# Kernel optimization log

Measured on AMD Instinct MI355X. Metric: run time of the kernel, lower is better.

## Reference

```python
import jax, jax.numpy as jnp
import numpy as np

N = 100000   # nodes
E = 1600000  # edges
G = 256      # graphs in batch
IN = 128     # in_feats
H = 64       # h_feats


def _xavier(k, shape):
    fan_in, fan_out = shape
    lim = float(np.sqrt(6.0 / (fan_in + fan_out)))
    return jax.random.uniform(k, shape, jnp.float32, -lim, lim)


def setup_inputs() -> dict:
    key = jax.random.key(0)
    ks = jax.random.split(key, 12)
    x = jax.random.normal(ks[0], (N, IN), jnp.float32)
    src = jax.random.randint(ks[1], (E,), 0, N)
    dst = jax.random.randint(ks[2], (E,), 0, N)
    ew = jax.random.uniform(ks[3], (E,), jnp.float32)
    gid = jnp.sort(jax.random.randint(ks[4], (N,), 0, G))
    def lin(k, fi, fo):
        kw, kb = jax.random.split(k)
        lim = float(np.sqrt(1.0 / fi))
        return (jax.random.uniform(kw, (fi, fo), jnp.float32, -lim, lim),
                jax.random.uniform(kb, (fo,), jnp.float32, -lim, lim))
    W1 = _xavier(ks[5], (IN, H)); b1 = jnp.zeros((H,), jnp.float32)
    W2 = _xavier(ks[6], (H, H));  b2 = jnp.zeros((H,), jnp.float32)
    W3 = _xavier(ks[7], (H, H));  b3 = jnp.zeros((H,), jnp.float32)
    Dw1, Db1 = lin(ks[8], H, 16)
    Dw2, Db2 = lin(ks[9], 16, 8)
    Dw3, Db3 = lin(ks[10], 8, 1)
    return {"x": x, "src": src, "dst": dst, "ew": ew, "gid": gid,
            "W1": W1, "b1": b1, "W2": W2, "b2": b2, "W3": W3, "b3": b3,
            "Dw1": Dw1, "Db1": Db1, "Dw2": Dw2, "Db2": Db2, "Dw3": Dw3, "Db3": Db3}


def reference(x, src, dst, ew, gid, W1, b1, W2, b2, W3, b3,
              Dw1, Db1, Dw2, Db2, Dw3, Db3):
    n = x.shape[0]
    # DGL GraphConv norm='both': unweighted degrees, clamped to >= 1
    deg_out = jnp.zeros((n,), x.dtype).at[src].add(1.0)
    deg_in = jnp.zeros((n,), x.dtype).at[dst].add(1.0)
    ns = jax.lax.rsqrt(jnp.maximum(deg_out, 1.0))  # src-side norm
    nd = jax.lax.rsqrt(jnp.maximum(deg_in, 1.0))   # dst-side norm

    def conv(h, W, b):
        # apply weight first (in >= out), then gather-scale-scatter
        h = (h * ns[:, None]) @ W                      # [N, out]
        m = h[src] * ew[:, None]                       # [E, out] edge messages
        agg = jnp.zeros((n, W.shape[1]), h.dtype).at[dst].add(m)
        return agg * nd[:, None] + b

    h = jax.nn.relu(conv(x, W1, b1))
    h = jax.nn.relu(conv(h, W2, b2))
    h = jax.nn.relu(conv(h, W3, b3))

    # mean_nodes: per-graph mean pooling
    counts = jnp.zeros((G,), h.dtype).at[gid].add(1.0)
    pooled = jnp.zeros((G, h.shape[1]), h.dtype).at[gid].add(h)
    pooled = pooled / jnp.maximum(counts, 1.0)[:, None]

    h = jax.nn.relu(pooled @ Dw1 + Db1)
    h = jax.nn.relu(h @ Dw2 + Db2)
    return jax.nn.sigmoid(h @ Dw3 + Db3)  # [G, 1]
```

## Files before the change

### kernel.cpp

```cpp
#include <hip/hip_runtime.h>
#include <math.h>

#define N_NODES 100000
#define N_EDGES 1600000
#define G_GRAPHS 256
#define IN_F 128
#define H_F 64

#define SCAN_CH 1024

#define HB 40
#define HCHUNK (N_EDGES / HB)
#define NWORDS (N_NODES / 4)
#define HNODES 25000
#define HWORDS (HNODES / 4)
#define HR 4

typedef unsigned int uint_t;
typedef unsigned short ushort_t;
typedef unsigned char uchar_t;
typedef __attribute__((ext_vector_type(8))) short short8;
typedef __attribute__((ext_vector_type(4))) float floatx4;
typedef __attribute__((ext_vector_type(2))) float floatx2;

__device__ __forceinline__ ushort_t f2bf(float f) {
  uint_t u = __float_as_uint(f);
  uint_t r = (u + 0x7fffu + ((u >> 16) & 1u)) >> 16;
  return (ushort_t)r;
}
__device__ __forceinline__ float bflo(uint_t u) { return __uint_as_float(u << 16); }
__device__ __forceinline__ uchar_t f2fp8(float f) {
  return (uchar_t)(__builtin_amdgcn_cvt_pk_fp8_f32(f, f, 0, false) & 0xff);
}

__global__ __launch_bounds__(1024) void hist8_kernel(
    const int* __restrict__ src, const int* __restrict__ dst,
    uint_t* __restrict__ p8dst, uint_t* __restrict__ p8src,
    uchar_t* __restrict__ rank8) {
  __shared__ uint_t h[HWORDS];
  const int a = blockIdx.x / (HR * HB);
  const int rem = blockIdx.x % (HR * HB);
  const int r = rem / HB;
  const int b = rem % HB;
  const uint_t rbase = (uint_t)(r * HNODES);

  for (int i = threadIdx.x; i < HWORDS; i += 1024) h[i] = 0u;
  __syncthreads();

  const int e0 = b * HCHUNK;
  const int* keys = a ? src : dst;
  const uint4* k4 = (const uint4*)(keys + e0);
  if (a == 0) {
    for (int i = threadIdx.x; i < HCHUNK / 4; i += 1024) {
      uint4 v = k4[i];
      int e = e0 + i * 4;
      uint_t t, sh;
      t = v.x - rbase; if (t < (uint_t)HNODES) { sh = (t & 3u) * 8u; rank8[e]     = (uchar_t)(atomicAdd(&h[t >> 2], 1u << sh) >> sh); }
      t = v.y - rbase; if (t < (uint_t)HNODES) { sh = (t & 3u) * 8u; rank8[e + 1] = (uchar_t)(atomicAdd(&h[t >> 2], 1u << sh) >> sh); }
      t = v.z - rbase; if (t < (uint_t)HNODES) { sh = (t & 3u) * 8u; rank8[e + 2] = (uchar_t)(atomicAdd(&h[t >> 2], 1u << sh) >> sh); }
      t = v.w - rbase; if (t < (uint_t)HNODES) { sh = (t & 3u) * 8u; rank8[e + 3] = (uchar_t)(atomicAdd(&h[t >> 2], 1u << sh) >> sh); }
    }
  } else {
    for (int i = threadIdx.x; i < HCHUNK / 4; i += 1024) {
      uint4 v = k4[i];
      uint_t t;
      t = v.x - rbase; if (t < (uint_t)HNODES) atomicAdd(&h[t >> 2], 1u << ((t & 3u) * 8u));
      t = v.y - rbase; if (t < (uint_t)HNODES) atomicAdd(&h[t >> 2], 1u << ((t & 3u) * 8u));
      t = v.z - rbase; if (t < (uint_t)HNODES) atomicAdd(&h[t >> 2], 1u << ((t & 3u) * 8u));
      t = v.w - rbase; if (t < (uint_t)HNODES) atomicAdd(&h[t >> 2], 1u << ((t & 3u) * 8u));
    }
  }
  __syncthreads();

  uint_t* outp = (a ? p8src : p8dst) + (size_t)b * NWORDS + r * HWORDS;
  for (int i = threadIdx.x; i < HWORDS; i += 1024) outp[i] = h[i];
}

__global__ __launch_bounds__(256) void scanA_kernel(
    const uint_t* __restrict__ p8dst, float* __restrict__ nd,
    int* __restrict__ row_ptr, int* __restrict__ bsums) {
  __shared__ int ts[256];
  const int tid = threadIdx.x;
  const int nodebase = blockIdx.x * SCAN_CH + tid * 4;
  const int w = nodebase >> 2;
  int c0 = 0, c1 = 0, c2 = 0, c3 = 0;
  if (nodebase < N_NODES) {
    for (int b = 0; b < HB; ++b) {
      uint_t x = p8dst[(size_t)b * NWORDS + w];
      c0 += (int)(x & 0xffu);
      c1 += (int)((x >> 8) & 0xffu);
      c2 += (int)((x >> 16) & 0xffu);
      c3 += (int)((x >> 24) & 0xffu);
    }
    ((float4*)nd)[w] = make_float4(
        rsqrtf(fmaxf((float)c0, 1.0f)), rsqrtf(fmaxf((float)c1, 1.0f)),
        rsqrtf(fmaxf((float)c2, 1.0f)), rsqrtf(fmaxf((float)c3, 1.0f)));
  }
  int s = c0 + c1 + c2 + c3;
  ts[tid] = s;
  __syncthreads();
  for (int off = 1; off < 256; off <<= 1) {
    int t = (tid >= off) ? ts[tid - off] : 0;
    __syncthreads();
    ts[tid] += t;
    __syncthreads();
  }
  int excl = (tid == 0) ? 0 : ts[tid - 1];
  if (nodebase < N_NODES)
    ((int4*)row_ptr)[w] = make_int4(excl, excl + c0, excl + c0 + c1,
                                    excl + c0 + c1 + c2);
  if (tid == 255) bsums[blockIdx.x] = ts[255];
}

__global__ __launch_bounds__(256) void scanB_kernel(int* __restrict__ bsums, int nb) {
  __shared__ int ts[256];
  const int tid = threadIdx.x;
  ts[tid] = (tid < nb) ? bsums[tid] : 0;
  __syncthreads();
  for (int off = 1; off < 256; off <<= 1) {
    int t = (tid >= off) ? ts[tid - off] : 0;
    __syncthreads();
    ts[tid] += t;
    __syncthreads();
  }
  if (tid < nb) bsums[tid] = (tid == 0) ? 0 : ts[tid - 1];
}

__global__ __launch_bounds__(256) void coff_kernel(
    const uint_t* __restrict__ p8dst, const int* __restrict__ bsums,
    const int* __restrict__ row_ptr, int* __restrict__ coff,
    int2* __restrict__ rc) {
  int v = blockIdx.x * blockDim.x + threadIdx.x;
  if (v >= N_NODES) return;
  int start = row_ptr[v] + bsums[v >> 10];
  int run = start;
  const int w = v >> 2, sh = (v & 3) * 8;
  for (int b = 0; b < HB; ++b) {
    int c = (int)((p8dst[(size_t)b * NWORDS + w] >> sh) & 0xffu);
    coff[(size_t)b * N_NODES + v] = run;
    run += c;
  }
  rc[v] = make_int2(start, run - start);
}

__global__ __launch_bounds__(256) void ns_kernel(
    const uint_t* __restrict__ p8src, float* __restrict__ ns) {
  int w = blockIdx.x * blockDim.x + threadIdx.x;
  if (w >= NWORDS) return;
  int c0 = 0, c1 = 0, c2 = 0, c3 = 0;
  for (int b = 0; b < HB; ++b) {
    uint_t x = p8src[(size_t)b * NWORDS + w];
    c0 += (int)(x & 0xffu);
    c1 += (int)((x >> 8) & 0xffu);
    c2 += (int)((x >> 16) & 0xffu);
    c3 += (int)((x >> 24) & 0xffu);
  }
  ((float4*)ns)[w] = make_float4(
      rsqrtf(fmaxf((float)c0, 1.0f)), rsqrtf(fmaxf((float)c1, 1.0f)),
      rsqrtf(fmaxf((float)c2, 1.0f)), rsqrtf(fmaxf((float)c3, 1.0f)));
}

#define PB 782
__global__ __launch_bounds__(256) void place_kernel(
    const int* __restrict__ src, const int* __restrict__ dst,
    const float* __restrict__ ew, const int* __restrict__ coff,
    const uchar_t* __restrict__ rank8, uint_t* __restrict__ csr) {
  int j = (blockIdx.x & 7) * PB + (blockIdx.x >> 3);
  int e = j * 256 + (int)threadIdx.x;
  if (e >= N_EDGES) return;
  int b = e / HCHUNK;
  int d = dst[e];
  int slot = coff[(size_t)b * N_NODES + d] + (int)rank8[e];
  uint_t entry = ((uint_t)(f2bf(ew[e]) & 0x7fff) << 17) | (uint_t)src[e];
  __builtin_nontemporal_store(entry, &csr[slot]);
}

template <int K, bool AFP32>
__global__ __launch_bounds__(256) void gemm_mfma_kernel(
    const void* __restrict__ Xin, const float* __restrict__ W,
    const float* __restrict__ ns, uchar_t* __restrict__ T, int ntiles) {
  constexpr int CH = K / 32;
  constexpr int WROW = K + 8;
  __shared__ __align__(16) ushort_t Wt[64 * WROW];
  const int tid = threadIdx.x;

  for (int i = tid; i < K * 64; i += 256) {
    int k = i >> 6, nn = i & 63;
    Wt[nn * WROW + k] = f2bf(W[i]);
  }
  __syncthreads();

  const int wave = tid >> 6;
  const int lane = tid & 63;
  const int tile = blockIdx.x * 4 + wave;
  if (tile >= ntiles) return;
  const int m = lane & 15;
  const int q = lane >> 4;
  const int node0 = tile * 16;

  short8 afrag[CH];
  if (AFP32) {
    const float* xr = (const float*)Xin + (size_t)(node0 + m) * K + q * 8;
#pragma unroll
    for (int c = 0; c < CH; ++c) {
      float4 xa = *(const float4*)(xr + c * 32);
      float4 xb = *(const float4*)(xr + c * 32 + 4);
      short8 a;
      a[0] = (short)f2bf(xa.x); a[1] = (short)f2bf(xa.y);
      a[2] = (short)f2bf(xa.z); a[3] = (short)f2bf(xa.w);
      a[4] = (short)f2bf(xb.x); a[5] = (short)f2bf(xb.y);
      a[6] = (short)f2bf(xb.z); a[7] = (short)f2bf(xb.w);
      afrag[c] = a;
    }
  } else {
    const ushort_t* xr = (const ushort_t*)Xin + (size_t)(node0 + m) * K + q * 8;
#pragma unroll
    for (int c = 0; c < CH; ++c)
      afrag[c] = *(const short8*)(xr + c * 32);
  }

  floatx4 acc[4];
#pragma unroll
  for (int t = 0; t < 4; ++t) acc[t] = (floatx4){0.f, 0.f, 0.f, 0.f};

#pragma unroll
  for (int t = 0; t < 4; ++t) {
    const ushort_t* wr = &Wt[(t * 16 + m) * WROW + q * 8];
#pragma unroll
    for (int c = 0; c < CH; ++c) {
      short8 bfrag = *(const short8*)(wr + c * 32);
      acc[t] = __builtin_amdgcn_mfma_f32_16x16x32_bf16(afrag[c], bfrag, acc[t], 0, 0, 0);
    }
  }

  float4 nsv = *(const float4*)(ns + node0 + q * 4);
  const float nsa[4] = {nsv.x, nsv.y, nsv.z, nsv.w};
#pragma unroll
  for (int t = 0; t < 4; ++t) {
#pragma unroll
    for (int r = 0; r < 4; ++r) {
      int node = node0 + q * 4 + r;
      T[(size_t)node * 64 + t * 16 + m] = f2fp8(acc[t][r] * nsa[r]);
    }
  }
}

__global__ __launch_bounds__(256) void gather_kernel(
    const uint_t* __restrict__ csr, const int2* __restrict__ rc,
    const uchar_t* __restrict__ T, const float* __restrict__ nd,
    const float* __restrict__ b, ushort_t* __restrict__ H, int n) {
  int id = blockIdx.x * blockDim.x + threadIdx.x;
  const int lane = threadIdx.x & 63;
  const int o = lane >> 3, l = lane & 7;
  int v = (id >> 6) * 8 + o;
  if (v >= n) return;
  int2 rcv = rc[v];
  const int start = rcv.x, cnt = rcv.y;

  float acc[8] = {0, 0, 0, 0, 0, 0, 0, 0};
  int k = 0;
  for (; k + 1 < cnt; k += 2) {
    uint_t e1 = csr[start + k];
    uint_t e2 = csr[start + k + 1];
    float w1 = __uint_as_float((e1 >> 17) << 16);
    float w2 = __uint_as_float((e2 >> 17) << 16);
    uint2 p1 = *((const uint2*)(T + (size_t)(e1 & 0x1ffffu) * 64) + l);
    uint2 p2 = *((const uint2*)(T + (size_t)(e2 & 0x1ffffu) * 64) + l);
    floatx2 a;
    a = __builtin_amdgcn_cvt_pk_f32_fp8(p1.x, false);
    acc[0] = fmaf(a.x, w1, acc[0]); acc[1] = fmaf(a.y, w1, acc[1]);
    a = __builtin_amdgcn_cvt_pk_f32_fp8(p1.x, true);
    acc[2] = fmaf(a.x, w1, acc[2]); acc[3] = fmaf(a.y, w1, acc[3]);
    a = __builtin_amdgcn_cvt_pk_f32_fp8(p1.y, false);
    acc[4] = fmaf(a.x, w1, acc[4]); acc[5] = fmaf(a.y, w1, acc[5]);
    a = __builtin_amdgcn_cvt_pk_f32_fp8(p1.y, true);
    acc[6] = fmaf(a.x, w1, acc[6]); acc[7] = fmaf(a.y, w1, acc[7]);
    a = __builtin_amdgcn_cvt_pk_f32_fp8(p2.x, false);
    acc[0] = fmaf(a.x, w2, acc[0]); acc[1] = fmaf(a.y, w2, acc[1]);
    a = __builtin_amdgcn_cvt_pk_f32_fp8(p2.x, true);
    acc[2] = fmaf(a.x, w2, acc[2]); acc[3] = fmaf(a.y, w2, acc[3]);
    a = __builtin_amdgcn_cvt_pk_f32_fp8(p2.y, false);
    acc[4] = fmaf(a.x, w2, acc[4]); acc[5] = fmaf(a.y, w2, acc[5]);
    a = __builtin_amdgcn_cvt_pk_f32_fp8(p2.y, true);
    acc[6] = fmaf(a.x, w2, acc[6]); acc[7] = fmaf(a.y, w2, acc[7]);
  }
  if (k < cnt) {
    uint_t e1 = csr[start + k];
    float w1 = __uint_as_float((e1 >> 17) << 16);
    uint2 p1 = *((const uint2*)(T + (size_t)(e1 & 0x1ffffu) * 64) + l);
    floatx2 a;
    a = __builtin_amdgcn_cvt_pk_f32_fp8(p1.x, false);
    acc[0] = fmaf(a.x, w1, acc[0]); acc[1] = fmaf(a.y, w1, acc[1]);
    a = __builtin_amdgcn_cvt_pk_f32_fp8(p1.x, true);
    acc[2] = fmaf(a.x, w1, acc[2]); acc[3] = fmaf(a.y, w1, acc[3]);
    a = __builtin_amdgcn_cvt_pk_f32_fp8(p1.y, false);
    acc[4] = fmaf(a.x, w1, acc[4]); acc[5] = fmaf(a.y, w1, acc[5]);
    a = __builtin_amdgcn_cvt_pk_f32_fp8(p1.y, true);
    acc[6] = fmaf(a.x, w1, acc[6]); acc[7] = fmaf(a.y, w1, acc[7]);
  }

  const float ndv = nd[v];
  float4 b0 = *(const float4*)&b[l * 8];
  float4 b1 = *(const float4*)&b[l * 8 + 4];
  uint4 ov;
  ov.x = (uint_t)f2bf(fmaxf(fmaf(acc[0], ndv, b0.x), 0.f)) |
         ((uint_t)f2bf(fmaxf(fmaf(acc[1], ndv, b0.y), 0.f)) << 16);
  ov.y = (uint_t)f2bf(fmaxf(fmaf(acc[2], ndv, b0.z), 0.f)) |
         ((uint_t)f2bf(fmaxf(fmaf(acc[3], ndv, b0.w), 0.f)) << 16);
  ov.z = (uint_t)f2bf(fmaxf(fmaf(acc[4], ndv, b1.x), 0.f)) |
         ((uint_t)f2bf(fmaxf(fmaf(acc[5], ndv, b1.y), 0.f)) << 16);
  ov.w = (uint_t)f2bf(fmaxf(fmaf(acc[6], ndv, b1.z), 0.f)) |
         ((uint_t)f2bf(fmaxf(fmaf(acc[7], ndv, b1.w), 0.f)) << 16);
  *((uint4*)(H + (size_t)v * 64) + l) = ov;
}

__global__ __launch_bounds__(256) void pool_mlp_kernel(
    const ushort_t* __restrict__ H, const int* __restrict__ gid,
    const float* __restrict__ Dw1, const float* __restrict__ Db1,
    const float* __restrict__ Dw2, const float* __restrict__ Db2,
    const float* __restrict__ Dw3, const float* __restrict__ Db3,
    float* __restrict__ out) {
  __shared__ float red[4][64];
  __shared__ float mean[64];
  __shared__ float h1s[16], h2s[8];
  const int g = blockIdx.x;
  int l = 0, r = N_NODES;
  while (l < r) { int m = (l + r) >> 1; if (gid[m] < g) l = m + 1; else r = m; }
  const int lo = l;
  r = N_NODES;
  while (l < r) { int m = (l + r) >> 1; if (gid[m] < g + 1) l = m + 1; else r = m; }
  const int hi = l;

  const int j = threadIdx.x & 63, s = threadIdx.x >> 6;
  float acc = 0.0f;
  for (int node = lo + s; node < hi; node += 4)
    acc += bflo((uint_t)H[(size_t)node * 64 + j]);
  red[s][j] = acc;
  __syncthreads();
  if (threadIdx.x < 64) {
    float inv = 1.0f / fmaxf((float)(hi - lo), 1.0f);
    mean[j] = (red[0][j] + red[1][j] + red[2][j] + red[3][j]) * inv;
  }
  __syncthreads();
  if (threadIdx.x < 16) {
    int o = threadIdx.x;
    float a = Db1[o];
#pragma unroll
    for (int k = 0; k < 64; ++k) a = fmaf(mean[k], Dw1[k * 16 + o], a);
    h1s[o] = fmaxf(a, 0.0f);
  }
  __syncthreads();
  if (threadIdx.x < 8) {
    int o = threadIdx.x;
    float a = Db2[o];
#pragma unroll
    for (int k = 0; k < 16; ++k) a = fmaf(h1s[k], Dw2[k * 8 + o], a);
    h2s[o] = fmaxf(a, 0.0f);
  }
  __syncthreads();
  if (threadIdx.x == 0) {
    float a = Db3[0];
#pragma unroll
    for (int k = 0; k < 8; ++k) a = fmaf(h2s[k], Dw3[k], a);
    out[g] = 1.0f / (1.0f + expf(-a));
  }
}

extern "C" void kernel_launch(void* const* d_in, const int* in_sizes, int n_in,
                              void* d_out, int out_size, void* d_ws, size_t ws_size,
                              hipStream_t stream) {
  const float* x   = (const float*)d_in[0];
  const int*   src = (const int*)  d_in[1];
  const int*   dst = (const int*)  d_in[2];
  const float* ew  = (const float*)d_in[3];
  const int*   gid = (const int*)  d_in[4];
  const float* W1  = (const float*)d_in[5];
  const float* b1  = (const float*)d_in[6];
  const float* W2  = (const float*)d_in[7];
  const float* b2  = (const float*)d_in[8];
  const float* W3  = (const float*)d_in[9];
  const float* b3  = (const float*)d_in[10];
  const float* Dw1 = (const float*)d_in[11];
  const float* Db1 = (const float*)d_in[12];
  const float* Dw2 = (const float*)d_in[13];
  const float* Db2 = (const float*)d_in[14];
  const float* Dw3 = (const float*)d_in[15];
  const float* Db3 = (const float*)d_in[16];
  float* out = (float*)d_out;

  char* ws = (char*)d_ws;
  uchar_t*  T8   = (uchar_t*)ws;
  ushort_t* Hb   = (ushort_t*)(T8 + (size_t)N_NODES * 64);
  uint_t*   csr  = (uint_t*)(Hb + (size_t)N_NODES * 64);
  uchar_t*  rank8= (uchar_t*)(csr + N_EDGES);
  uint_t*   p8dst= (uint_t*)(rank8 + N_EDGES);
  uint_t*   p8src= p8dst + (size_t)HB * NWORDS;
  float*    ns   = (float*)(p8src + (size_t)HB * NWORDS);
  float*    nd   = ns + N_NODES;
  int*      row_ptr = (int*)(nd + N_NODES);
  int*      bsums   = row_ptr + N_NODES;
  int2*     rc      = (int2*)(bsums + 128);
  int*      coff   = (int*)T8;

  const int NTILES  = N_NODES / 16;
  const int NB_N    = (N_NODES + 255) / 256;
  const int NB_SCAN = (N_NODES + SCAN_CH - 1) / SCAN_CH;
  const int NB_W    = (NWORDS + 255) / 256;
  const int NB_HIST = 2 * HR * HB;
  const int NB_GEMM = (NTILES + 3) / 4;
  const int NB_GATH = (N_NODES * 8 + 255) / 256;
  const int NB_PLACE= 8 * PB;

  hist8_kernel<<<NB_HIST, 1024, 0, stream>>>(src, dst, p8dst, p8src, rank8);
  scanA_kernel<<<NB_SCAN, 256, 0, stream>>>(p8dst, nd, row_ptr, bsums);
  scanB_kernel<<<1, 256, 0, stream>>>(bsums, NB_SCAN);
  coff_kernel<<<NB_N, 256, 0, stream>>>(p8dst, bsums, row_ptr, coff, rc);
  ns_kernel<<<NB_W, 256, 0, stream>>>(p8src, ns);
  place_kernel<<<NB_PLACE, 256, 0, stream>>>(src, dst, ew, coff, rank8, csr);

  gemm_mfma_kernel<IN_F, true><<<NB_GEMM, 256, 0, stream>>>(x, W1, ns, T8, NTILES);
  gather_kernel<<<NB_GATH, 256, 0, stream>>>(csr, rc, T8, nd, b1, Hb, N_NODES);
  gemm_mfma_kernel<H_F, false><<<NB_GEMM, 256, 0, stream>>>(Hb, W2, ns, T8, NTILES);
  gather_kernel<<<NB_GATH, 256, 0, stream>>>(csr, rc, T8, nd, b2, Hb, N_NODES);
  gemm_mfma_kernel<H_F, false><<<NB_GEMM, 256, 0, stream>>>(Hb, W3, ns, T8, NTILES);
  gather_kernel<<<NB_GATH, 256, 0, stream>>>(csr, rc, T8, nd, b3, Hb, N_NODES);

  pool_mlp_kernel<<<G_GRAPHS, 256, 0, stream>>>(Hb, gid, Dw1, Db1, Dw2, Db2,
                                                Dw3, Db3, out);
}
```

Before: 338.1 us.

## Partition CSR placement by destination range and pack gather FMAs

The place kernel now has each of 8 block groups scan a span of edges with vectorized dst loads and handle only edges whose destination falls in that group's node range. This localizes scattered coff reads and csr writes to a smaller address window, likely intended for L2/MALL locality, at the cost of reading dst eight times. Separately, the gather kernel's accumulators become float2 vectors so the compiler can emit packed FMA instructions, reducing ALU instruction count.

Measured after the change: 369.9 us. 1.09x slower.

```diff
diff --git a/kernel.cpp b/kernel.cpp
--- a/kernel.cpp
+++ b/kernel.cpp
@@ -15,6 +15,10 @@
 #define HNODES 25000
 #define HWORDS (HNODES / 4)
 #define HR 4
+
+#define PRNODES (N_NODES / 8)
+#define PSPAN 4096
+#define PBLK ((N_EDGES + PSPAN - 1) / PSPAN)
 
 typedef unsigned int uint_t;
 typedef unsigned short ushort_t;
@@ -160,19 +164,30 @@
       rsqrtf(fmaxf((float)c2, 1.0f)), rsqrtf(fmaxf((float)c3, 1.0f)));
 }
 
-#define PB 782
 __global__ __launch_bounds__(256) void place_kernel(
     const int* __restrict__ src, const int* __restrict__ dst,
     const float* __restrict__ ew, const int* __restrict__ coff,
     const uchar_t* __restrict__ rank8, uint_t* __restrict__ csr) {
-  int j = (blockIdx.x & 7) * PB + (blockIdx.x >> 3);
-  int e = j * 256 + (int)threadIdx.x;
-  if (e >= N_EDGES) return;
-  int b = e / HCHUNK;
-  int d = dst[e];
-  int slot = coff[(size_t)b * N_NODES + d] + (int)rank8[e];
-  uint_t entry = ((uint_t)(f2bf(ew[e]) & 0x7fff) << 17) | (uint_t)src[e];
-  __builtin_nontemporal_store(entry, &csr[slot]);
+  const int r = blockIdx.x & 7;
+  const int blk = blockIdx.x >> 3;
+  const uint_t rbase = (uint_t)(r * PRNODES);
+  const int e0 = blk * PSPAN;
+  const int eend = min(e0 + PSPAN, N_EDGES);
+  for (int i = e0 + (int)threadIdx.x * 4; i < eend; i += 256 * 4) {
+    uint4 d4 = *(const uint4*)(dst + i);
+#pragma unroll
+    for (int k = 0; k < 4; ++k) {
+      uint_t dv = (k == 0 ? d4.x : k == 1 ? d4.y : k == 2 ? d4.z : d4.w);
+      uint_t t = dv - rbase;
+      if (t < (uint_t)PRNODES) {
+        int e = i + k;
+        int b = e / HCHUNK;
+        int slot = coff[(size_t)b * N_NODES + dv] + (int)rank8[e];
+        uint_t entry = ((uint_t)(f2bf(ew[e]) & 0x7fff) << 17) | (uint_t)src[e];
+        __builtin_nontemporal_store(entry, &csr[slot]);
+      }
+    }
+  }
 }
 
 template <int K, bool AFP32>
@@ -257,60 +272,49 @@
   int2 rcv = rc[v];
   const int start = rcv.x, cnt = rcv.y;
 
-  float acc[8] = {0, 0, 0, 0, 0, 0, 0, 0};
+  floatx2 acc2[4];
+#pragma unroll
+  for (int i = 0; i < 4; ++i) acc2[i] = (floatx2){0.f, 0.f};
+
   int k = 0;
   for (; k + 1 < cnt; k += 2) {
     uint_t e1 = csr[start + k];
     uint_t e2 = csr[start + k + 1];
-    float w1 = __uint_as_float((e1 >> 17) << 16);
-    float w2 = __uint_as_float((e2 >> 17) << 16);
+    floatx2 w1; w1.x = w1.y = __uint_as_float((e1 >> 17) << 16);
+    floatx2 w2; w2.x = w2.y = __uint_as_float((e2 >> 17) << 16);
     uint2 p1 = *((const uint2*)(T + (size_t)(e1 & 0x1ffffu) * 64) + l);
     uint2 p2 = *((const uint2*)(T + (size_t)(e2 & 0x1ffffu) * 64) + l);
-    floatx2 a;
-    a = __builtin_amdgcn_cvt_pk_f32_fp8(p1.x, false);
-    acc[0] = fmaf(a.x, w1, acc[0]); acc[1] = fmaf(a.y, w1, acc[1]);
-    a = __builtin_amdgcn_cvt_pk_f32_fp8(p1.x, true);
-    acc[2] = fmaf(a.x, w1, acc[2]); acc[3] = fmaf(a.y, w1, acc[3]);
-    a = __builtin_amdgcn_cvt_pk_f32_fp8(p1.y, false);
-    acc[4] = fmaf(a.x, w1, acc[4]); acc[5] = fmaf(a.y, w1, acc[5]);
-    a = __builtin_amdgcn_cvt_pk_f32_fp8(p1.y, true);
-    acc[6] = fmaf(a.x, w1, acc[6]); acc[7] = fmaf(a.y, w1, acc[7]);
-    a = __builtin_amdgcn_cvt_pk_f32_fp8(p2.x, false);
-    acc[0] = fmaf(a.x, w2, acc[0]); acc[1] = fmaf(a.y, w2, acc[1]);
-    a = __builtin_amdgcn_cvt_pk_f32_fp8(p2.x, true);
-    acc[2] = fmaf(a.x, w2, acc[2]); acc[3] = fmaf(a.y, w2, acc[3]);
-    a = __builtin_amdgcn_cvt_pk_f32_fp8(p2.y, false);
-    acc[4] = fmaf(a.x, w2, acc[4]); acc[5] = fmaf(a.y, w2, acc[5]);
-    a = __builtin_amdgcn_cvt_pk_f32_fp8(p2.y, true);
-    acc[6] = fmaf(a.x, w2, acc[6]); acc[7] = fmaf(a.y, w2, acc[7]);
+    acc2[0] = __builtin_amdgcn_cvt_pk_f32_fp8(p1.x, false) * w1 + acc2[0];
+    acc2[1] = __builtin_amdgcn_cvt_pk_f32_fp8(p1.x, true)  * w1 + acc2[1];
+    acc2[2] = __builtin_amdgcn_cvt_pk_f32_fp8(p1.y, false) * w1 + acc2[2];
+    acc2[3] = __builtin_amdgcn_cvt_pk_f32_fp8(p1.y, true)  * w1 + acc2[3];
+    acc2[0] = __builtin_amdgcn_cvt_pk_f32_fp8(p2.x, false) * w2 + acc2[0];
+    acc2[1] = __builtin_amdgcn_cvt_pk_f32_fp8(p2.x, true)  * w2 + acc2[1];
+    acc2[2] = __builtin_amdgcn_cvt_pk_f32_fp8(p2.y, false) * w2 + acc2[2];
+    acc2[3] = __builtin_amdgcn_cvt_pk_f32_fp8(p2.y, true)  * w2 + acc2[3];
   }
   if (k < cnt) {
     uint_t e1 = csr[start + k];
-    float w1 = __uint_as_float((e1 >> 17) << 16);
+    floatx2 w1; w1.x = w1.y = __uint_as_float((e1 >> 17) << 16);
     uint2 p1 = *((const uint2*)(T + (size_t)(e1 & 0x1ffffu) * 64) + l);
-    floatx2 a;
-    a = __builtin_amdgcn_cvt_pk_f32_fp8(p1.x, false);
-    acc[0] = fmaf(a.x, w1, acc[0]); acc[1] = fmaf(a.y, w1, acc[1]);
-    a = __builtin_amdgcn_cvt_pk_f32_fp8(p1.x, true);
-    acc[2] = fmaf(a.x, w1, acc[2]); acc[3] = fmaf(a.y, w1, acc[3]);
-    a = __builtin_amdgcn_cvt_pk_f32_fp8(p1.y, false);
-    acc[4] = fmaf(a.x, w1, acc[4]); acc[5] = fmaf(a.y, w1, acc[5]);
-    a = __builtin_amdgcn_cvt_pk_f32_fp8(p1.y, true);
-    acc[6] = fmaf(a.x, w1, acc[6]); acc[7] = fmaf(a.y, w1, acc[7]);
+    acc2[0] = __builtin_amdgcn_cvt_pk_f32_fp8(p1.x, false) * w1 + acc2[0];
+    acc2[1] = __builtin_amdgcn_cvt_pk_f32_fp8(p1.x, true)  * w1 + acc2[1];
+    acc2[2] = __builtin_amdgcn_cvt_pk_f32_fp8(p1.y, false) * w1 + acc2[2];
+    acc2[3] = __builtin_amdgcn_cvt_pk_f32_fp8(p1.y, true)  * w1 + acc2[3];
   }
 
   const float ndv = nd[v];
   float4 b0 = *(const float4*)&b[l * 8];
   float4 b1 = *(const float4*)&b[l * 8 + 4];
   uint4 ov;
-  ov.x = (uint_t)f2bf(fmaxf(fmaf(acc[0], ndv, b0.x), 0.f)) |
-         ((uint_t)f2bf(fmaxf(fmaf(acc[1], ndv, b0.y), 0.f)) << 16);
-  ov.y = (uint_t)f2bf(fmaxf(fmaf(acc[2], ndv, b0.z), 0.f)) |
-         ((uint_t)f2bf(fmaxf(fmaf(acc[3], ndv, b0.w), 0.f)) << 16);
-  ov.z = (uint_t)f2bf(fmaxf(fmaf(acc[4], ndv, b1.x), 0.f)) |
-         ((uint_t)f2bf(fmaxf(fmaf(acc[5], ndv, b1.y), 0.f)) << 16);
-  ov.w = (uint_t)f2bf(fmaxf(fmaf(acc[6], ndv, b1.z), 0.f)) |
-         ((uint_t)f2bf(fmaxf(fmaf(acc[7], ndv, b1.w), 0.f)) << 16);
+  ov.x = (uint_t)f2bf(fmaxf(fmaf(acc2[0].x, ndv, b0.x), 0.f)) |
+         ((uint_t)f2bf(fmaxf(fmaf(acc2[0].y, ndv, b0.y), 0.f)) << 16);
+  ov.y = (uint_t)f2bf(fmaxf(fmaf(acc2[1].x, ndv, b0.z), 0.f)) |
+         ((uint_t)f2bf(fmaxf(fmaf(acc2[1].y, ndv, b0.w), 0.f)) << 16);
+  ov.z = (uint_t)f2bf(fmaxf(fmaf(acc2[2].x, ndv, b1.x), 0.f)) |
+         ((uint_t)f2bf(fmaxf(fmaf(acc2[2].y, ndv, b1.y), 0.f)) << 16);
+  ov.w = (uint_t)f2bf(fmaxf(fmaf(acc2[3].x, ndv, b1.z), 0.f)) |
+         ((uint_t)f2bf(fmaxf(fmaf(acc2[3].y, ndv, b1.w), 0.f)) << 16);
   *((uint4*)(H + (size_t)v * 64) + l) = ov;
 }
 
@@ -409,7 +413,7 @@
   const int NB_HIST = 2 * HR * HB;
   const int NB_GEMM = (NTILES + 3) / 4;
   const int NB_GATH = (N_NODES * 8 + 255) / 256;
-  const int NB_PLACE= 8 * PB;
+  const int NB_PLACE= 8 * PBLK;
 
   hist8_kernel<<<NB_HIST, 1024, 0, stream>>>(src, dst, p8dst, p8src, rank8);
   scanA_kernel<<<NB_SCAN, 256, 0, stream>>>(p8dst, nd, row_ptr, bsums);
```

## Build CSR via region bucketing and per-region LDS placement

Applied to the files above, without the earlier changes.

Replaces the destination histogram, the multi-kernel prefix scan, the coff computation and the scattered place kernel with a two-pass scheme. Edges are first bucketed by 625-node destination region into fixed-capacity buckets. One block per region then counts, scans and places its edges in LDS and writes a contiguous CSR slice, computing rc and nd along the way. This cuts kernel launches and scattered global writes. The price is a hard bucket capacity that silently drops edges if a region gets more than 11000, and only 160 blocks in the placement stage.

New measurement: 323.6 us. 1.04x faster.

```diff
diff --git a/kernel.cpp b/kernel.cpp
--- a/kernel.cpp
+++ b/kernel.cpp
@@ -6,8 +6,6 @@
 #define G_GRAPHS 256
 #define IN_F 128
 #define H_F 64
-
-#define SCAN_CH 1024
 
 #define HB 40
 #define HCHUNK (N_EDGES / HB)
@@ -16,6 +14,12 @@
 #define HWORDS (HNODES / 4)
 #define HR 4
 
+#define NREG 160
+#define REG_NODES 625
+#define BUCKET_CAP 11000
+#define BSPAN 6400
+#define NB_BUCKET (N_EDGES / BSPAN)
+
 typedef unsigned int uint_t;
 typedef unsigned short ushort_t;
 typedef unsigned char uchar_t;
@@ -33,114 +37,29 @@
   return (uchar_t)(__builtin_amdgcn_cvt_pk_fp8_f32(f, f, 0, false) & 0xff);
 }
 
-__global__ __launch_bounds__(1024) void hist8_kernel(
-    const int* __restrict__ src, const int* __restrict__ dst,
-    uint_t* __restrict__ p8dst, uint_t* __restrict__ p8src,
-    uchar_t* __restrict__ rank8) {
+__global__ __launch_bounds__(1024) void hist8_src_kernel(
+    const int* __restrict__ src, uint_t* __restrict__ p8src) {
   __shared__ uint_t h[HWORDS];
-  const int a = blockIdx.x / (HR * HB);
-  const int rem = blockIdx.x % (HR * HB);
-  const int r = rem / HB;
-  const int b = rem % HB;
+  const int r = blockIdx.x / HB;
+  const int b = blockIdx.x % HB;
   const uint_t rbase = (uint_t)(r * HNODES);
 
   for (int i = threadIdx.x; i < HWORDS; i += 1024) h[i] = 0u;
   __syncthreads();
 
-  const int e0 = b * HCHUNK;
-  const int* keys = a ? src : dst;
-  const uint4* k4 = (const uint4*)(keys + e0);
-  if (a == 0) {
-    for (int i = threadIdx.x; i < HCHUNK / 4; i += 1024) {
-      uint4 v = k4[i];
-      int e = e0 + i * 4;
-      uint_t t, sh;
-      t = v.x - rbase; if (t < (uint_t)HNODES) { sh = (t & 3u) * 8u; rank8[e]     = (uchar_t)(atomicAdd(&h[t >> 2], 1u << sh) >> sh); }
-      t = v.y - rbase; if (t < (uint_t)HNODES) { sh = (t & 3u) * 8u; rank8[e + 1] = (uchar_t)(atomicAdd(&h[t >> 2], 1u << sh) >> sh); }
-      t = v.z - rbase; if (t < (uint_t)HNODES) { sh = (t & 3u) * 8u; rank8[e + 2] = (uchar_t)(atomicAdd(&h[t >> 2], 1u << sh) >> sh); }
-      t = v.w - rbase; if (t < (uint_t)HNODES) { sh = (t & 3u) * 8u; rank8[e + 3] = (uchar_t)(atomicAdd(&h[t >> 2], 1u << sh) >> sh); }
-    }
-  } else {
-    for (int i = threadIdx.x; i < HCHUNK / 4; i += 1024) {
-      uint4 v = k4[i];
-      uint_t t;
-      t = v.x - rbase; if (t < (uint_t)HNODES) atomicAdd(&h[t >> 2], 1u << ((t & 3u) * 8u));
-      t = v.y - rbase; if (t < (uint_t)HNODES) atomicAdd(&h[t >> 2], 1u << ((t & 3u) * 8u));
-      t = v.z - rbase; if (t < (uint_t)HNODES) atomicAdd(&h[t >> 2], 1u << ((t & 3u) * 8u));
-      t = v.w - rbase; if (t < (uint_t)HNODES) atomicAdd(&h[t >> 2], 1u << ((t & 3u) * 8u));
-    }
-  }
-  __syncthreads();
-
-  uint_t* outp = (a ? p8src : p8dst) + (size_t)b * NWORDS + r * HWORDS;
+  const uint4* k4 = (const uint4*)(src + b * HCHUNK);
+  for (int i = threadIdx.x; i < HCHUNK / 4; i += 1024) {
+    uint4 v = k4[i];
+    uint_t t;
+    t = v.x - rbase; if (t < (uint_t)HNODES) atomicAdd(&h[t >> 2], 1u << ((t & 3u) * 8u));
+    t = v.y - rbase; if (t < (uint_t)HNODES) atomicAdd(&h[t >> 2], 1u << ((t & 3u) * 8u));
+    t = v.z - rbase; if (t < (uint_t)HNODES) atomicAdd(&h[t >> 2], 1u << ((t & 3u) * 8u));
+    t = v.w - rbase; if (t < (uint_t)HNODES) atomicAdd(&h[t >> 2], 1u << ((t & 3u) * 8u));
+  }
+  __syncthreads();
+
+  uint_t* outp = p8src + (size_t)b * NWORDS + r * HWORDS;
   for (int i = threadIdx.x; i < HWORDS; i += 1024) outp[i] = h[i];
-}
-
-__global__ __launch_bounds__(256) void scanA_kernel(
-    const uint_t* __restrict__ p8dst, float* __restrict__ nd,
-    int* __restrict__ row_ptr, int* __restrict__ bsums) {
-  __shared__ int ts[256];
-  const int tid = threadIdx.x;
-  const int nodebase = blockIdx.x * SCAN_CH + tid * 4;
-  const int w = nodebase >> 2;
-  int c0 = 0, c1 = 0, c2 = 0, c3 = 0;
-  if (nodebase < N_NODES) {
-    for (int b = 0; b < HB; ++b) {
-      uint_t x = p8dst[(size_t)b * NWORDS + w];
-      c0 += (int)(x & 0xffu);
-      c1 += (int)((x >> 8) & 0xffu);
-      c2 += (int)((x >> 16) & 0xffu);
-      c3 += (int)((x >> 24) & 0xffu);
-    }
-    ((float4*)nd)[w] = make_float4(
-        rsqrtf(fmaxf((float)c0, 1.0f)), rsqrtf(fmaxf((float)c1, 1.0f)),
-        rsqrtf(fmaxf((float)c2, 1.0f)), rsqrtf(fmaxf((float)c3, 1.0f)));
-  }
-  int s = c0 + c1 + c2 + c3;
-  ts[tid] = s;
-  __syncthreads();
-  for (int off = 1; off < 256; off <<= 1) {
-    int t = (tid >= off) ? ts[tid - off] : 0;
-    __syncthreads();
-    ts[tid] += t;
-    __syncthreads();
-  }
-  int excl = (tid == 0) ? 0 : ts[tid - 1];
-  if (nodebase < N_NODES)
-    ((int4*)row_ptr)[w] = make_int4(excl, excl + c0, excl + c0 + c1,
-                                    excl + c0 + c1 + c2);
-  if (tid == 255) bsums[blockIdx.x] = ts[255];
-}
-
-__global__ __launch_bounds__(256) void scanB_kernel(int* __restrict__ bsums, int nb) {
-  __shared__ int ts[256];
-  const int tid = threadIdx.x;
-  ts[tid] = (tid < nb) ? bsums[tid] : 0;
-  __syncthreads();
-  for (int off = 1; off < 256; off <<= 1) {
-    int t = (tid >= off) ? ts[tid - off] : 0;
-    __syncthreads();
-    ts[tid] += t;
-    __syncthreads();
-  }
-  if (tid < nb) bsums[tid] = (tid == 0) ? 0 : ts[tid - 1];
-}
-
-__global__ __launch_bounds__(256) void coff_kernel(
-    const uint_t* __restrict__ p8dst, const int* __restrict__ bsums,
-    const int* __restrict__ row_ptr, int* __restrict__ coff,
-    int2* __restrict__ rc) {
-  int v = blockIdx.x * blockDim.x + threadIdx.x;
-  if (v >= N_NODES) return;
-  int start = row_ptr[v] + bsums[v >> 10];
-  int run = start;
-  const int w = v >> 2, sh = (v & 3) * 8;
-  for (int b = 0; b < HB; ++b) {
-    int c = (int)((p8dst[(size_t)b * NWORDS + w] >> sh) & 0xffu);
-    coff[(size_t)b * N_NODES + v] = run;
-    run += c;
-  }
-  rc[v] = make_int2(start, run - start);
 }
 
 __global__ __launch_bounds__(256) void ns_kernel(
@@ -160,19 +79,109 @@
       rsqrtf(fmaxf((float)c2, 1.0f)), rsqrtf(fmaxf((float)c3, 1.0f)));
 }
 
-#define PB 782
-__global__ __launch_bounds__(256) void place_kernel(
+__global__ __launch_bounds__(256) void bucket_kernel(
     const int* __restrict__ src, const int* __restrict__ dst,
-    const float* __restrict__ ew, const int* __restrict__ coff,
-    const uchar_t* __restrict__ rank8, uint_t* __restrict__ csr) {
-  int j = (blockIdx.x & 7) * PB + (blockIdx.x >> 3);
-  int e = j * 256 + (int)threadIdx.x;
-  if (e >= N_EDGES) return;
-  int b = e / HCHUNK;
-  int d = dst[e];
-  int slot = coff[(size_t)b * N_NODES + d] + (int)rank8[e];
-  uint_t entry = ((uint_t)(f2bf(ew[e]) & 0x7fff) << 17) | (uint_t)src[e];
-  __builtin_nontemporal_store(entry, &csr[slot]);
+    const float* __restrict__ ew, int* __restrict__ bcnt,
+    uint2* __restrict__ bucket) {
+  __shared__ uint_t rl[BSPAN];
+  __shared__ int cnt[NREG];
+  __shared__ int cur[NREG];
+  const int e0 = blockIdx.x * BSPAN;
+
+  for (int i = threadIdx.x; i < NREG; i += 256) cnt[i] = 0;
+  __syncthreads();
+
+  for (int i = threadIdx.x; i < BSPAN; i += 256) {
+    uint_t d = (uint_t)dst[e0 + i];
+    uint_t r = d / REG_NODES;
+    uint_t loc = d - r * REG_NODES;
+    rl[i] = (r << 16) | loc;
+    atomicAdd(&cnt[r], 1);
+  }
+  __syncthreads();
+
+  for (int i = threadIdx.x; i < NREG; i += 256)
+    cur[i] = atomicAdd(&bcnt[i], cnt[i]);
+  __syncthreads();
+
+  for (int i = threadIdx.x; i < BSPAN; i += 256) {
+    uint_t v = rl[i];
+    uint_t r = v >> 16, loc = v & 0xffffu;
+    int pos = atomicAdd(&cur[r], 1);
+    if (pos < BUCKET_CAP)
+      bucket[(size_t)r * BUCKET_CAP + pos] = make_uint2(
+          (loc << 17) | (uint_t)src[e0 + i], __float_as_uint(ew[e0 + i]));
+  }
+}
+
+__global__ __launch_bounds__(256) void region_place_kernel(
+    const uint2* __restrict__ bucket, const int* __restrict__ bcnt,
+    uint_t* __restrict__ csr, int2* __restrict__ rc, float* __restrict__ nd) {
+  __shared__ uint_t staged[BUCKET_CAP];
+  __shared__ int cnt[REG_NODES];
+  __shared__ int sc[REG_NODES];
+  __shared__ int ts[256];
+  const int r = blockIdx.x;
+  const int tid = threadIdx.x;
+  const int nE = min(bcnt[r], BUCKET_CAP);
+
+  ts[tid] = (tid < NREG) ? min(bcnt[tid], BUCKET_CAP) : 0;
+  for (int i = tid; i < REG_NODES; i += 256) cnt[i] = 0;
+  __syncthreads();
+  for (int off = 1; off < 256; off <<= 1) {
+    int t = (tid >= off) ? ts[tid - off] : 0;
+    __syncthreads();
+    ts[tid] += t;
+    __syncthreads();
+  }
+  const int csr_base = (r == 0) ? 0 : ts[r - 1];
+  __syncthreads();
+
+  const uint2* bk = bucket + (size_t)r * BUCKET_CAP;
+  for (int i = tid; i < nE; i += 256) atomicAdd(&cnt[bk[i].x >> 17], 1);
+  __syncthreads();
+
+  const int loc0 = tid * 3;
+  int c3v[3], s = 0;
+#pragma unroll
+  for (int k = 0; k < 3; ++k) {
+    int idx = loc0 + k;
+    c3v[k] = (idx < REG_NODES) ? cnt[idx] : 0;
+    s += c3v[k];
+  }
+  __syncthreads();
+  ts[tid] = s;
+  __syncthreads();
+  for (int off = 1; off < 256; off <<= 1) {
+    int t = (tid >= off) ? ts[tid - off] : 0;
+    __syncthreads();
+    ts[tid] += t;
+    __syncthreads();
+  }
+  int run = (tid == 0) ? 0 : ts[tid - 1];
+#pragma unroll
+  for (int k = 0; k < 3; ++k) {
+    int idx = loc0 + k;
+    if (idx < REG_NODES) {
+      sc[idx] = run;
+      int v = r * REG_NODES + idx;
+      rc[v] = make_int2(csr_base + run, c3v[k]);
+      nd[v] = rsqrtf(fmaxf((float)c3v[k], 1.0f));
+      run += c3v[k];
+    }
+  }
+  __syncthreads();
+
+  for (int i = tid; i < nE; i += 256) {
+    uint2 e = bk[i];
+    uint_t loc = e.x >> 17;
+    int pos = atomicAdd(&sc[loc], 1);
+    staged[pos] = ((uint_t)(f2bf(__uint_as_float(e.y)) & 0x7fff) << 17) |
+                  (e.x & 0x1ffffu);
+  }
+  __syncthreads();
+
+  for (int i = tid; i < nE; i += 256) csr[csr_base + i] = staged[i];
 }
 
 template <int K, bool AFP32>
@@ -389,34 +398,27 @@
   float* out = (float*)d_out;
 
   char* ws = (char*)d_ws;
-  uchar_t*  T8   = (uchar_t*)ws;
-  ushort_t* Hb   = (ushort_t*)(T8 + (size_t)N_NODES * 64);
-  uint_t*   csr  = (uint_t*)(Hb + (size_t)N_NODES * 64);
-  uchar_t*  rank8= (uchar_t*)(csr + N_EDGES);
-  uint_t*   p8dst= (uint_t*)(rank8 + N_EDGES);
-  uint_t*   p8src= p8dst + (size_t)HB * NWORDS;
-  float*    ns   = (float*)(p8src + (size_t)HB * NWORDS);
-  float*    nd   = ns + N_NODES;
-  int*      row_ptr = (int*)(nd + N_NODES);
-  int*      bsums   = row_ptr + N_NODES;
-  int2*     rc      = (int2*)(bsums + 128);
-  int*      coff   = (int*)T8;
+  uchar_t*  T8    = (uchar_t*)ws;
+  ushort_t* Hb    = (ushort_t*)(T8 + (size_t)N_NODES * 64);
+  uint_t*   csr   = (uint_t*)(Hb + (size_t)N_NODES * 64);
+  uint_t*   p8src = (uint_t*)(csr + N_EDGES);
+  float*    ns    = (float*)(p8src + (size_t)HB * NWORDS);
+  float*    nd    = ns + N_NODES;
+  int2*     rc    = (int2*)(nd + N_NODES);
+  int*      bcnt  = (int*)(rc + N_NODES);
+  uint2*    bucket = (uint2*)T8;
 
   const int NTILES  = N_NODES / 16;
-  const int NB_N    = (N_NODES + 255) / 256;
-  const int NB_SCAN = (N_NODES + SCAN_CH - 1) / SCAN_CH;
   const int NB_W    = (NWORDS + 255) / 256;
-  const int NB_HIST = 2 * HR * HB;
+  const int NB_HIST = HR * HB;
   const int NB_GEMM = (NTILES + 3) / 4;
   const int NB_GATH = (N_NODES * 8 + 255) / 256;
-  const int NB_PLACE= 8 * PB;
-
-  hist8_kernel<<<NB_HIST, 1024, 0, stream>>>(src, dst, p8dst, p8src, rank8);
-  scanA_kernel<<<NB_SCAN, 256, 0, stream>>>(p8dst, nd, row_ptr, bsums);
-  scanB_kernel<<<1, 256, 0, stream>>>(bsums, NB_SCAN);
-  coff_kernel<<<NB_N, 256, 0, stream>>>(p8dst, bsums, row_ptr, coff, rc);
+
+  hipMemsetAsync(bcnt, 0, NREG * sizeof(int), stream);
+  bucket_kernel<<<NB_BUCKET, 256, 0, stream>>>(src, dst, ew, bcnt, bucket);
+  hist8_src_kernel<<<NB_HIST, 1024, 0, stream>>>(src, p8src);
   ns_kernel<<<NB_W, 256, 0, stream>>>(p8src, ns);
-  place_kernel<<<NB_PLACE, 256, 0, stream>>>(src, dst, ew, coff, rank8, csr);
+  region_place_kernel<<<NREG, 256, 0, stream>>>(bucket, bcnt, csr, rc, nd);
 
   gemm_mfma_kernel<IN_F, true><<<NB_GEMM, 256, 0, stream>>>(x, W1, ns, T8, NTILES);
   gather_kernel<<<NB_GATH, 256, 0, stream>>>(csr, rc, T8, nd, b1, Hb, N_NODES);
```
